# Kernel optimization log

Hardware: AMD Instinct MI355X
Metric: run time of the kernel (lower is better)

## Reference

```python
import jax, jax.numpy as jnp
import numpy as np

NEG_SLOPE = 0.2
EPS = 1e-16


def add_self_loops(edge_index, num_nodes):
    loops = jnp.arange(num_nodes, dtype=edge_index.dtype)
    return jnp.concatenate([edge_index, jnp.stack([loops, loops])], axis=1)


def gat_conv(x, edge_index, W, att_src, att_dst, bias, concat):
    # PyG GATConv: linear -> per-head attention logits -> segment softmax over
    # incoming edges of each destination node -> weighted scatter-add.
    N = x.shape[0]
    H, C = att_src.shape
    ei = add_self_loops(edge_index, N)
    src, dst = ei[0], ei[1]
    h = (x @ W).reshape(N, H, C)                      # [N,H,C]
    a_src = jnp.einsum('nhc,hc->nh', h, att_src)       # [N,H]
    a_dst = jnp.einsum('nhc,hc->nh', h, att_dst)       # [N,H]
    logits = jax.nn.leaky_relu(a_src[src] + a_dst[dst], NEG_SLOPE)  # [E,H]
    m = jax.ops.segment_max(logits, dst, num_segments=N)            # [N,H]
    e = jnp.exp(logits - m[dst])
    s = jax.ops.segment_sum(e, dst, num_segments=N)                 # [N,H]
    alpha = e / (s[dst] + EPS)                                      # [E,H]
    out = jax.ops.segment_sum(h[src] * alpha[:, :, None], dst, num_segments=N)  # [N,H,C]
    out = out.reshape(N, H * C) if concat else out.mean(axis=1)
    return out + bias


def setup_inputs() -> dict:
    key = jax.random.key(0)
    ks = jax.random.split(key, 10)
    N, E, F_in, Hd, heads, F_out = 50000, 800000, 128, 32, 4, 64
    return {
        'x': jax.random.normal(ks[0], (N, F_in), jnp.float32),
        'edge_index': jax.random.randint(ks[1], (2, E), 0, N, jnp.int64),
        'W1': jax.random.normal(ks[2], (F_in, heads * Hd), jnp.float32) * 0.1,
        'att_src1': jax.random.normal(ks[3], (heads, Hd), jnp.float32) * 0.1,
        'att_dst1': jax.random.normal(ks[4], (heads, Hd), jnp.float32) * 0.1,
        'bias1': jax.random.normal(ks[5], (heads * Hd,), jnp.float32) * 0.1,
        'W2': jax.random.normal(ks[6], (heads * Hd, heads * F_out), jnp.float32) * 0.1,
        'att_src2': jax.random.normal(ks[7], (heads, F_out), jnp.float32) * 0.1,
        'att_dst2': jax.random.normal(ks[8], (heads, F_out), jnp.float32) * 0.1,
        'bias2': jax.random.normal(ks[9], (F_out,), jnp.float32) * 0.1,
    }


def reference(x, edge_index, W1, att_src1, att_dst1, bias1, W2, att_src2, att_dst2, bias2):
    h = gat_conv(x, edge_index, W1, att_src1, att_dst1, bias1, concat=True)
    h = jax.nn.elu(h)  # dropout p=0.0 / eval mode -> identity
    out = gat_conv(h, edge_index, W2, att_src2, att_dst2, bias2, concat=False)
    return out
```

## Files before the change

### kernel.cpp

```cpp
#include <hip/hip_runtime.h>

typedef unsigned int uint;
typedef unsigned short ushort;


__device__ __forceinline__ float leaky(float x) { return x >= 0.f ? x : 0.2f * x; }
__device__ __forceinline__ float b2f(ushort h) { return __uint_as_float(((uint)h) << 16); }
__device__ __forceinline__ ushort f2b(float f) {
    uint u = __float_as_uint(f);
    return (ushort)((u + 0x7FFF + ((u >> 16) & 1)) >> 16);
}

#if defined(__has_builtin)
#if __has_builtin(__builtin_amdgcn_fdot2_f32_bf16)
#define HAS_DOT2 1
#endif
#endif
#ifndef HAS_DOT2
#define HAS_DOT2 0
#endif

#if HAS_DOT2
typedef __bf16 bf16v2 __attribute__((ext_vector_type(2)));
__device__ __forceinline__ float dot2bf(uint h2, uint w2, float c) {
    return __builtin_amdgcn_fdot2_f32_bf16(__builtin_bit_cast(bf16v2, h2),
                                           __builtin_bit_cast(bf16v2, w2), c, false);
}
#define DOT2PAIR(hE, hE1, wpk, a0, a1)                                  \
    a0 = dot2bf(__builtin_amdgcn_perm(hE, hE1, 0x01000504), wpk, a0);   \
    a1 = dot2bf(__builtin_amdgcn_perm(hE, hE1, 0x03020706), wpk, a1);
#else
#define DOT2PAIR(hE, hE1, wpk, a0, a1)                                  \
    {                                                                   \
        float wlo = __uint_as_float((wpk) << 16);                       \
        float whi = __uint_as_float((wpk) & 0xffff0000u);               \
        a0 = fmaf(wlo, __uint_as_float((hE) << 16), a0);                \
        a1 = fmaf(wlo, __uint_as_float((hE) & 0xffff0000u), a1);        \
        a0 = fmaf(whi, __uint_as_float((hE1) << 16), a0);               \
        a1 = fmaf(whi, __uint_as_float((hE1) & 0xffff0000u), a1);       \
    }
#endif

__device__ __forceinline__ int detect_bf_local(const void* xin) {
    __shared__ int s_sane;
    if (threadIdx.x == 0) s_sane = 0;
    __syncthreads();
    ushort v = ((const ushort*)xin)[2 * threadIdx.x];
    int ex = (v >> 7) & 0xFF;
    if (v == 0 || (ex >= 100 && ex <= 135)) atomicAdd(&s_sane, 1);
    __syncthreads();
    return s_sane >= 230;
}
__device__ __forceinline__ int detect_is64_local(const int* ei) {
    __shared__ int s_odd;
    if (threadIdx.x == 0) s_odd = 0;
    __syncthreads();
    if (threadIdx.x < 64 && ei[2 * threadIdx.x + 1] != 0) atomicOr(&s_odd, 1);
    __syncthreads();
    return s_odd == 0;
}

__device__ __forceinline__ float rdf(const void* p_, int i, int bf) {
    return bf ? b2f(((const ushort*)p_)[i]) : ((const float*)p_)[i];
}

__device__ __forceinline__ int edge_dst(const int* __restrict__ ei, int E, int e, int is64) {
    return (e >= E) ? (e - E) : (is64 ? ei[2 * E + 2 * e] : ei[E + e]);
}

__global__ void prep_kernel(const void* __restrict__ x, const void* __restrict__ W1,
                            const void* __restrict__ as1, const void* __restrict__ ad1,
                            const void* __restrict__ b1, const void* __restrict__ b2,
                            const void* __restrict__ W2, const void* __restrict__ as2,
                            const void* __restrict__ ad2, const int* __restrict__ ei,
                            int E, int ET,
                            ushort* __restrict__ W1T, float* __restrict__ att1,
                            float* __restrict__ b1f, float* __restrict__ b2f_,
                            float* __restrict__ w2t8, ushort* __restrict__ W2sT,
                            int* __restrict__ flagI, int* __restrict__ flagF,
                            int* __restrict__ bcnt) {
    int b = blockIdx.x, t = threadIdx.x;
    if (b < 64) {
        int bf = detect_bf_local(x);
        int i = b * 256 + t;
        int k = i >> 7, n = i & 127;
        W1T[n * 128 + k] = bf ? ((const ushort*)W1)[i] : f2b(((const float*)W1)[i]);
        return;
    }
    b -= 64;
    if (b == 0) {
        int bf = detect_bf_local(x);
        int is64 = detect_is64_local(ei);
        if (t == 0) { *flagF = bf; *flagI = is64; }
        for (int i = t; i < 512; i += 256) {
            if (i < 128)      att1[i] = rdf(as1, i, bf);
            else if (i < 256) att1[i] = rdf(ad1, i - 128, bf);
            else if (i < 384) b1f[i - 256] = rdf(b1, i - 256, bf);
            else if (i < 448) b2f_[i - 384] = rdf(b2, i - 384, bf);
        }
        return;
    }
    b -= 1;
    if (b < 4) {
        int bf = detect_bf_local(x);
        int idx = b * 256 + t;
        int o = idx >> 7, k = idx & 127, h = o & 3;
        const void* att = (o < 4) ? as2 : ad2;
        float s = 0.f;
        for (int c = 0; c < 64; ++c) s += rdf(W2, k * 256 + h * 64 + c, bf) * rdf(att, h * 64 + c, bf);
        w2t8[o * 128 + k] = s;
        return;
    }
    b -= 4;
    if (b < 128) {
        int bf = detect_bf_local(x);
        int idx = b * 256 + t;
        int c = idx >> 9, hk = idx & 511;
        int h = hk >> 7, k = hk & 127;
        W2sT[c * 512 + hk] = f2b(0.25f * rdf(W2, k * 256 + h * 64 + c, bf));
        return;
    }
    b -= 128;
    {
        int is64 = detect_is64_local(ei);
        __shared__ int bins[256];
        bins[t] = 0;
        __syncthreads();
        int base = b * 4096;
        for (int i = 0; i < 16; ++i) {
            int e = base + i * 256 + t;
            if (e < ET) atomicAdd(&bins[edge_dst(ei, E, e, is64) >> 8], 1);
        }
        __syncthreads();
        if (bins[t]) atomicAdd(&bcnt[t], bins[t]);
    }
}

typedef __attribute__((ext_vector_type(8))) short bf16x8;
typedef __attribute__((ext_vector_type(4))) float floatx4;

__device__ __forceinline__ void gemm1_body(
    int blk, const void* __restrict__ xraw, const int* __restrict__ flagF,
    const ushort* __restrict__ BT, ushort* __restrict__ C,
    const float* __restrict__ att, float4* __restrict__ asrc4, float4* __restrict__ adst4,
    int M) {
    constexpr int K = 128, NT = 8;
    int lane = threadIdx.x & 63, wv = threadIdx.x >> 6;
    int row0 = (blk * 4 + wv) * 16;
    if (row0 >= M) return;
    int m = lane & 15, quad = lane >> 4;
    int rowa = min(row0 + m, M - 1);
    bf16x8 af[4];
    if (*flagF) {
        const bf16x8* arow = (const bf16x8*)((const ushort*)xraw + (size_t)rowa * K);
#pragma unroll
        for (int kk = 0; kk < 4; ++kk) af[kk] = arow[4 * kk + quad];
    } else {
        const float4* arw = (const float4*)((const float*)xraw + (size_t)rowa * K);
#pragma unroll
        for (int kk = 0; kk < 4; ++kk) {
            float4 fa = arw[2 * (4 * kk + quad)];
            float4 fb = arw[2 * (4 * kk + quad) + 1];
            bf16x8 tv;
            tv[0] = (short)f2b(fa.x); tv[1] = (short)f2b(fa.y);
            tv[2] = (short)f2b(fa.z); tv[3] = (short)f2b(fa.w);
            tv[4] = (short)f2b(fb.x); tv[5] = (short)f2b(fb.y);
            tv[6] = (short)f2b(fb.z); tv[7] = (short)f2b(fb.w);
            af[kk] = tv;
        }
    }
    floatx4 acc[NT] = {};
#pragma unroll
    for (int nt = 0; nt < NT; ++nt) {
        const bf16x8* brow = (const bf16x8*)(BT + (size_t)(nt * 16 + m) * K);
#pragma unroll
        for (int kk = 0; kk < 4; ++kk)
            acc[nt] = __builtin_amdgcn_mfma_f32_16x16x32_bf16(af[kk], brow[4 * kk + quad], acc[nt], 0, 0, 0);
    }
#pragma unroll
    for (int nt = 0; nt < NT; ++nt)
#pragma unroll
        for (int r = 0; r < 4; ++r) {
            int row = row0 + quad * 4 + r;
            if (row < M) C[(size_t)row * 128 + nt * 16 + m] = f2b(acc[nt][r]);
        }
    float attS[NT], attD[NT];
#pragma unroll
    for (int nt = 0; nt < NT; ++nt) { attS[nt] = att[nt * 16 + m]; attD[nt] = att[128 + nt * 16 + m]; }
#pragma unroll
    for (int r = 0; r < 4; ++r) {
        float ps[4] = {0, 0, 0, 0}, pd[4] = {0, 0, 0, 0};
#pragma unroll
        for (int nt = 0; nt < NT; ++nt) {
            int h = nt / 2;
            ps[h] = fmaf(acc[nt][r], attS[nt], ps[h]);
            pd[h] = fmaf(acc[nt][r], attD[nt], pd[h]);
        }
#pragma unroll
        for (int off = 1; off < 16; off <<= 1) {
#pragma unroll
            for (int h = 0; h < 4; ++h) {
                ps[h] += __shfl_xor(ps[h], off, 64);
                pd[h] += __shfl_xor(pd[h], off, 64);
            }
        }
        int row = row0 + quad * 4 + r;
        if (m == 0 && row < M) {
            asrc4[row] = make_float4(ps[0], ps[1], ps[2], ps[3]);
            adst4[row] = make_float4(pd[0], pd[1], pd[2], pd[3]);
        }
    }
}

__global__ __launch_bounds__(256) void partg_kernel(
    const int* __restrict__ ei, int E, int ET, const int* __restrict__ flagI,
    const int* __restrict__ bcnt, int* __restrict__ gofs, uint* __restrict__ ebuf,
    int NBUK, int npart,
    const void* __restrict__ xraw, const int* __restrict__ flagF,
    const ushort* __restrict__ BT, ushort* __restrict__ C, const float* __restrict__ att,
    float4* __restrict__ asrc4, float4* __restrict__ adst4, int M) {
    if ((int)blockIdx.x >= npart) {
        gemm1_body(blockIdx.x - npart, xraw, flagF, BT, C, att, asrc4, adst4, M);
        return;
    }
    __shared__ uint stage[8192];
    __shared__ int cnt_s[256], sc[256], sc2[256], lbase[257], cur[256], gb[256];
    int t = threadIdx.x;
    int base = blockIdx.x * 8192;
    cnt_s[t] = 0;
    __syncthreads();
    int is64 = *flagI;
    uint pk[32];
    short bk[32];
#pragma unroll
    for (int i = 0; i < 32; ++i) {
        int e = base + i * 256 + t;
        if (e < ET) {
            int src, dst;
            if (e >= E) { src = dst = e - E; }
            else if (is64) { src = ei[2 * e]; dst = ei[2 * E + 2 * e]; }
            else           { src = ei[e];     dst = ei[E + e]; }
            pk[i] = (uint)src | ((uint)dst << 16);
            bk[i] = (short)(dst >> 8);
            atomicAdd(&cnt_s[bk[i]], 1);
        } else bk[i] = -1;
    }
    __syncthreads();
    int v = cnt_s[t];
    int v2 = (t < NBUK) ? bcnt[t] : 0;
    sc[t] = v;
    sc2[t] = v2;
    __syncthreads();
    for (int off = 1; off < 256; off <<= 1) {
        int a  = (t >= off) ? sc[t - off]  : 0;
        int a2 = (t >= off) ? sc2[t - off] : 0;
        __syncthreads();
        sc[t] += a; sc2[t] += a2;
        __syncthreads();
    }
    lbase[t + 1] = sc[t];
    cur[t] = sc[t] - v;
    int bbx = sc2[t] - v2;
    if (t == 0) lbase[0] = 0;
    __syncthreads();
#pragma unroll
    for (int i = 0; i < 32; ++i)
        if (bk[i] >= 0) {
            int slot = atomicAdd(&cur[bk[i]], 1);
            stage[slot] = pk[i];
        }
    __syncthreads();
    if (t < NBUK) {
        int c = lbase[t + 1] - lbase[t];
        if (c > 0) gb[t] = bbx + atomicAdd(&gofs[t], c);
    }
    __syncthreads();
    int total = lbase[256];
    for (int i = t; i < total; i += 256) {
        int lo = 0, hi = 255;
        while (lo < hi) { int mid = (lo + hi + 1) >> 1; if (lbase[mid] <= i) lo = mid; else hi = mid - 1; }
        ebuf[gb[lo] + (i - lbase[lo])] = stage[i];
    }
}

__global__ __launch_bounds__(256) void bfinal_kernel(const uint* __restrict__ ebuf,
                                                     const int* __restrict__ bcnt,
                                                     int* __restrict__ rowptr,
                                                     int* __restrict__ ecol, int N, int NBUK) {
    __shared__ int hist[2048], cur2[2048], ws[4], bb[256];
    int b = blockIdx.x, t = threadIdx.x;
    int lane = t & 63, wid = t >> 6;
    int d0 = b << 8;
    bb[t] = (t < NBUK) ? bcnt[t] : 0;
#pragma unroll
    for (int j = 0; j < 8; ++j) hist[t * 8 + j] = 0;
    __syncthreads();
    for (int off = 1; off < 256; off <<= 1) {
        int a = (t >= off) ? bb[t - off] : 0;
        __syncthreads();
        bb[t] += a;
        __syncthreads();
    }
    int s = (b == 0) ? 0 : bb[b - 1];
    int e2 = bb[b];
    int total = bb[255];
    for (int i = s + t; i < e2; i += 256) {
        uint pk = ebuf[i];
        int key = (((int)(pk >> 16) - d0) << 3) | (int)((pk & 0xffffu) >> 13);
        atomicAdd(&hist[key], 1);
    }
    __syncthreads();
    int loc[8];
    int v = 0;
#pragma unroll
    for (int j = 0; j < 8; ++j) { loc[j] = v; v += hist[t * 8 + j]; }
    int incl = v;
#pragma unroll
    for (int off = 1; off < 64; off <<= 1) {
        int a = __shfl_up(incl, off, 64);
        if (lane >= off) incl += a;
    }
    if (lane == 63) ws[wid] = incl;
    __syncthreads();
    if (t == 0) {
        int acc = 0;
        for (int j = 0; j < 4; ++j) { int x = ws[j]; ws[j] = acc; acc += x; }
    }
    __syncthreads();
    int excl = incl - v + ws[wid];
    int d = d0 + t;
    if (d < N) rowptr[d] = s + excl;
#pragma unroll
    for (int j = 0; j < 8; ++j) cur2[t * 8 + j] = s + excl + loc[j];
    if (b == NBUK - 1 && t == 0) rowptr[N] = total;
    __syncthreads();
    for (int i = s + t; i < e2; i += 256) {
        uint pk = ebuf[i];
        int key = (((int)(pk >> 16) - d0) << 3) | (int)((pk & 0xffffu) >> 13);
        int pos = atomicAdd(&cur2[key], 1);
        ecol[pos] = (int)(pk & 0xffffu);
    }
}

__global__ void hist_kernel(const int* __restrict__ ei, int E, int N,
                            const int* __restrict__ flag, int* __restrict__ deg) {
    int e = blockIdx.x * blockDim.x + threadIdx.x;
    if (e >= E + N) return;
    atomicAdd(&deg[edge_dst(ei, E, e, *flag)], 1);
}
__global__ void scatter_kernel(const int* __restrict__ ei, int E, int N,
                               const int* __restrict__ flag, const int* __restrict__ rowptr,
                               int* __restrict__ cnt, int* __restrict__ ecol) {
    int e = blockIdx.x * blockDim.x + threadIdx.x;
    if (e >= E + N) return;
    int src, dst;
    if (e >= E) { src = dst = e - E; }
    else if (*flag) { src = ei[2 * e]; dst = ei[2 * E + 2 * e]; }
    else            { src = ei[e];     dst = ei[E + e]; }
    int pos = rowptr[dst] + atomicAdd(&cnt[dst], 1);
    ecol[pos] = src;
}
__global__ __launch_bounds__(1024) void scan1_kernel(const int* __restrict__ deg,
                                                     int* __restrict__ tmp,
                                                     int* __restrict__ bsum, int n) {
    __shared__ int ws[16];
    int tid = threadIdx.x, lane = tid & 63, wid = tid >> 6;
    int i = blockIdx.x * 1024 + tid;
    int v = (i < n) ? deg[i] : 0;
    int incl = v;
#pragma unroll
    for (int off = 1; off < 64; off <<= 1) {
        int t2 = __shfl_up(incl, off, 64);
        if (lane >= off) incl += t2;
    }
    if (lane == 63) ws[wid] = incl;
    __syncthreads();
    if (tid < 16) {
        int wv_ = ws[tid], winc = wv_;
#pragma unroll
        for (int off = 1; off < 16; off <<= 1) {
            int t2 = __shfl_up(winc, off, 16);
            if (tid >= off) winc += t2;
        }
        ws[tid] = winc - wv_;
    }
    __syncthreads();
    int excl = incl - v + ws[wid];
    if (i < n) tmp[i] = excl;
    if (tid == 1023) bsum[blockIdx.x] = excl + v;
}
__global__ void scan2_kernel(int* __restrict__ bsum, int nb) {
    int lane = threadIdx.x;
    int v = (lane < nb) ? bsum[lane] : 0;
    int incl = v;
    for (int off = 1; off < 64; off <<= 1) {
        int t = __shfl_up(incl, off, 64);
        if (lane >= off) incl += t;
    }
    int total = __shfl(incl, nb - 1, 64);
    if (lane < nb) bsum[lane] = incl - v;
    if (lane == 0) bsum[nb] = total;
}
__global__ void scan3_kernel(const int* __restrict__ tmp, const int* __restrict__ bsum,
                             int* __restrict__ rowptr, int* __restrict__ cnt, int n, int nb) {
    int i = blockIdx.x * blockDim.x + threadIdx.x;
    if (i > n) return;
    rowptr[i] = (i == n) ? bsum[nb] : tmp[i] + bsum[i >> 10];
    if (i < n) cnt[i] = 0;
}

__global__ __launch_bounds__(256) void gemm1_kernel(
    const void* __restrict__ xraw, const int* __restrict__ flagF,
    const ushort* __restrict__ BT, ushort* __restrict__ C,
    const float* __restrict__ att, float4* __restrict__ asrc4, float4* __restrict__ adst4, int M) {
    gemm1_body(blockIdx.x, xraw, flagF, BT, C, att, asrc4, adst4, M);
}

__global__ __launch_bounds__(256) void agg1_kernel(
    const ushort* __restrict__ hsrc, const float4* __restrict__ a_src4,
    const float4* __restrict__ a_dst4, const int* __restrict__ rowptr,
    const int* __restrict__ ecol, const float* __restrict__ bias,
    const float* __restrict__ w2t8, uint4* __restrict__ outz,
    float4* __restrict__ asrc2, float4* __restrict__ adst2, int N) {
    constexpr int SH = 7;
    __shared__ __align__(16) ushort elds[4][4][4][20];
    int lane = threadIdx.x & 63, wv = threadIdx.x >> 6;
    int q = lane >> 4, c = lane & 15, qbase = q << 4;
    int n = blockIdx.x * 16 + wv * 4 + q;
    bool nv = n < N;
    int start = 0, end = 0;
    if (nv) { start = rowptr[n]; end = rowptr[n + 1]; }
    int deg = end - start;
    float4 ad = nv ? a_dst4[n] : make_float4(0.f, 0.f, 0.f, 0.f);
    int hh = c >> 2;
    uint laneoff = (uint)c * 8;
    float acc[8] = {};
    float ss0 = 0.f, ss1 = 0.f, ss2 = 0.f, ss3 = 0.f;

    for (int cs = 0; cs < deg; cs += 16) {
        int len = min(16, deg - cs);
        bool v = c < len;
        int sv = v ? ecol[start + cs + c] : 0;
        float4 as = a_src4[sv];
        float e0 = v ? __expf(fminf(leaky(as.x + ad.x), 60.f)) : 0.f;
        float e1 = v ? __expf(fminf(leaky(as.y + ad.y), 60.f)) : 0.f;
        float e2 = v ? __expf(fminf(leaky(as.z + ad.z), 60.f)) : 0.f;
        float e3 = v ? __expf(fminf(leaky(as.w + ad.w), 60.f)) : 0.f;
        ushort r0 = f2b(e0), r1 = f2b(e1), r2 = f2b(e2), r3 = f2b(e3);
        elds[wv][0][q][c] = r0; elds[wv][1][q][c] = r1;
        elds[wv][2][q][c] = r2; elds[wv][3][q][c] = r3;
        ss0 += b2f(r0); ss1 += b2f(r1); ss2 += b2f(r2); ss3 += b2f(r3);
        for (int e = 0; e < len; e += 4) {
            int s0 = __shfl(sv, qbase + e + 0, 64);
            int s1 = __shfl(sv, qbase + e + 1, 64);
            int s2 = __shfl(sv, qbase + e + 2, 64);
            int s3 = __shfl(sv, qbase + e + 3, 64);
            uint2 w = *(const uint2*)&elds[wv][hh][q][e];
            uint4 h0 = *(const uint4*)(hsrc + (((uint)s0) << SH) + laneoff);
            uint4 h1 = *(const uint4*)(hsrc + (((uint)s1) << SH) + laneoff);
            uint4 h2 = *(const uint4*)(hsrc + (((uint)s2) << SH) + laneoff);
            uint4 h3 = *(const uint4*)(hsrc + (((uint)s3) << SH) + laneoff);
            DOT2PAIR(h0.x, h1.x, w.x, acc[0], acc[1]); DOT2PAIR(h0.y, h1.y, w.x, acc[2], acc[3]);
            DOT2PAIR(h0.z, h1.z, w.x, acc[4], acc[5]); DOT2PAIR(h0.w, h1.w, w.x, acc[6], acc[7]);
            DOT2PAIR(h2.x, h3.x, w.y, acc[0], acc[1]); DOT2PAIR(h2.y, h3.y, w.y, acc[2], acc[3]);
            DOT2PAIR(h2.z, h3.z, w.y, acc[4], acc[5]); DOT2PAIR(h2.w, h3.w, w.y, acc[6], acc[7]);
        }
    }
#pragma unroll
    for (int off = 1; off < 16; off <<= 1) {
        ss0 += __shfl_xor(ss0, off, 64); ss1 += __shfl_xor(ss1, off, 64);
        ss2 += __shfl_xor(ss2, off, 64); ss3 += __shfl_xor(ss3, off, 64);
    }
    if (!nv) return;
    float ih = (hh == 0) ? 1.f / (ss0 + 1e-16f) : (hh == 1) ? 1.f / (ss1 + 1e-16f)
             : (hh == 2) ? 1.f / (ss2 + 1e-16f) : 1.f / (ss3 + 1e-16f);
    float4 bA = ((const float4*)bias)[2 * c], bB = ((const float4*)bias)[2 * c + 1];
    float o[8];
    o[0] = acc[0] * ih + bA.x; o[1] = acc[1] * ih + bA.y;
    o[2] = acc[2] * ih + bA.z; o[3] = acc[3] * ih + bA.w;
    o[4] = acc[4] * ih + bB.x; o[5] = acc[5] * ih + bB.y;
    o[6] = acc[6] * ih + bB.z; o[7] = acc[7] * ih + bB.w;
#pragma unroll
    for (int j = 0; j < 8; ++j) o[j] = o[j] > 0.f ? o[j] : __expf(o[j]) - 1.f;
    uint4 pk;
    pk.x = (uint)f2b(o[0]) | ((uint)f2b(o[1]) << 16);
    pk.y = (uint)f2b(o[2]) | ((uint)f2b(o[3]) << 16);
    pk.z = (uint)f2b(o[4]) | ((uint)f2b(o[5]) << 16);
    pk.w = (uint)f2b(o[6]) | ((uint)f2b(o[7]) << 16);
    outz[(size_t)n * 16 + c] = pk;

    float po[8];
#pragma unroll
    for (int oo = 0; oo < 8; ++oo) {
        float4 wA = ((const float4*)(w2t8 + oo * 128))[2 * c];
        float4 wB = ((const float4*)(w2t8 + oo * 128))[2 * c + 1];
        po[oo] = o[0] * wA.x + o[1] * wA.y + o[2] * wA.z + o[3] * wA.w
               + o[4] * wB.x + o[5] * wB.y + o[6] * wB.z + o[7] * wB.w;
    }
#pragma unroll
    for (int off = 1; off < 16; off <<= 1)
#pragma unroll
        for (int oo = 0; oo < 8; ++oo) po[oo] += __shfl_xor(po[oo], off, 64);
    if (c == 0) {
        asrc2[n] = make_float4(po[0], po[1], po[2], po[3]);
        adst2[n] = make_float4(po[4], po[5], po[6], po[7]);
    }
}

__global__ __launch_bounds__(256) void agg2_kernel(
    const ushort* __restrict__ hsrc, const float4* __restrict__ a_src4,
    const float4* __restrict__ a_dst4, const int* __restrict__ rowptr,
    const int* __restrict__ ecol, const ushort* __restrict__ W2sT,
    const float* __restrict__ b2, float* __restrict__ outp, int N) {
    constexpr int SH = 7;
    __shared__ __align__(16) ushort elds[4][4][4][20];
    __shared__ __align__(16) ushort lds_a[16][520];
    int lane = threadIdx.x & 63, wv = threadIdx.x >> 6;
    int q = lane >> 4, c = lane & 15, qbase = q << 4;
    int n = blockIdx.x * 16 + wv * 4 + q;
    bool nv = n < N;
    int start = 0, end = 0;
    if (nv) { start = rowptr[n]; end = rowptr[n + 1]; }
    int deg = end - start;
    float4 ad = nv ? a_dst4[n] : make_float4(0.f, 0.f, 0.f, 0.f);
    uint laneoff = (uint)c * 8;
    float a0_[8] = {}, a1_[8] = {}, a2_[8] = {}, a3_[8] = {};
    float ss0 = 0.f, ss1 = 0.f, ss2 = 0.f, ss3 = 0.f;

    for (int cs = 0; cs < deg; cs += 16) {
        int len = min(16, deg - cs);
        bool v = c < len;
        int sv = v ? ecol[start + cs + c] : 0;
        float4 as = a_src4[sv];
        float e0 = v ? __expf(fminf(leaky(as.x + ad.x), 60.f)) : 0.f;
        float e1 = v ? __expf(fminf(leaky(as.y + ad.y), 60.f)) : 0.f;
        float e2 = v ? __expf(fminf(leaky(as.z + ad.z), 60.f)) : 0.f;
        float e3 = v ? __expf(fminf(leaky(as.w + ad.w), 60.f)) : 0.f;
        ushort r0 = f2b(e0), r1 = f2b(e1), r2 = f2b(e2), r3 = f2b(e3);
        elds[wv][0][q][c] = r0; elds[wv][1][q][c] = r1;
        elds[wv][2][q][c] = r2; elds[wv][3][q][c] = r3;
        ss0 += b2f(r0); ss1 += b2f(r1); ss2 += b2f(r2); ss3 += b2f(r3);
        for (int e = 0; e < len; e += 4) {
            int s0 = __shfl(sv, qbase + e + 0, 64);
            int s1 = __shfl(sv, qbase + e + 1, 64);
            int s2 = __shfl(sv, qbase + e + 2, 64);
            int s3 = __shfl(sv, qbase + e + 3, 64);
            uint2 w0 = *(const uint2*)&elds[wv][0][q][e];
            uint2 w1 = *(const uint2*)&elds[wv][1][q][e];
            uint2 w2 = *(const uint2*)&elds[wv][2][q][e];
            uint2 w3 = *(const uint2*)&elds[wv][3][q][e];
            uint4 h0 = *(const uint4*)(hsrc + (((uint)s0) << SH) + laneoff);
            uint4 h1 = *(const uint4*)(hsrc + (((uint)s1) << SH) + laneoff);
            uint4 h2 = *(const uint4*)(hsrc + (((uint)s2) << SH) + laneoff);
            uint4 h3 = *(const uint4*)(hsrc + (((uint)s3) << SH) + laneoff);
            DOT2PAIR(h0.x, h1.x, w0.x, a0_[0], a0_[1]); DOT2PAIR(h0.y, h1.y, w0.x, a0_[2], a0_[3]);
            DOT2PAIR(h0.z, h1.z, w0.x, a0_[4], a0_[5]); DOT2PAIR(h0.w, h1.w, w0.x, a0_[6], a0_[7]);
            DOT2PAIR(h0.x, h1.x, w1.x, a1_[0], a1_[1]); DOT2PAIR(h0.y, h1.y, w1.x, a1_[2], a1_[3]);
            DOT2PAIR(h0.z, h1.z, w1.x, a1_[4], a1_[5]); DOT2PAIR(h0.w, h1.w, w1.x, a1_[6], a1_[7]);
            DOT2PAIR(h0.x, h1.x, w2.x, a2_[0], a2_[1]); DOT2PAIR(h0.y, h1.y, w2.x, a2_[2], a2_[3]);
            DOT2PAIR(h0.z, h1.z, w2.x, a2_[4], a2_[5]); DOT2PAIR(h0.w, h1.w, w2.x, a2_[6], a2_[7]);
            DOT2PAIR(h0.x, h1.x, w3.x, a3_[0], a3_[1]); DOT2PAIR(h0.y, h1.y, w3.x, a3_[2], a3_[3]);
            DOT2PAIR(h0.z, h1.z, w3.x, a3_[4], a3_[5]); DOT2PAIR(h0.w, h1.w, w3.x, a3_[6], a3_[7]);
            DOT2PAIR(h2.x, h3.x, w0.y, a0_[0], a0_[1]); DOT2PAIR(h2.y, h3.y, w0.y, a0_[2], a0_[3]);
            DOT2PAIR(h2.z, h3.z, w0.y, a0_[4], a0_[5]); DOT2PAIR(h2.w, h3.w, w0.y, a0_[6], a0_[7]);
            DOT2PAIR(h2.x, h3.x, w1.y, a1_[0], a1_[1]); DOT2PAIR(h2.y, h3.y, w1.y, a1_[2], a1_[3]);
            DOT2PAIR(h2.z, h3.z, w1.y, a1_[4], a1_[5]); DOT2PAIR(h2.w, h3.w, w1.y, a1_[6], a1_[7]);
            DOT2PAIR(h2.x, h3.x, w2.y, a2_[0], a2_[1]); DOT2PAIR(h2.y, h3.y, w2.y, a2_[2], a2_[3]);
            DOT2PAIR(h2.z, h3.z, w2.y, a2_[4], a2_[5]); DOT2PAIR(h2.w, h3.w, w2.y, a2_[6], a2_[7]);
            DOT2PAIR(h2.x, h3.x, w3.y, a3_[0], a3_[1]); DOT2PAIR(h2.y, h3.y, w3.y, a3_[2], a3_[3]);
            DOT2PAIR(h2.z, h3.z, w3.y, a3_[4], a3_[5]); DOT2PAIR(h2.w, h3.w, w3.y, a3_[6], a3_[7]);
        }
    }
#pragma unroll
    for (int off = 1; off < 16; off <<= 1) {
        ss0 += __shfl_xor(ss0, off, 64); ss1 += __shfl_xor(ss1, off, 64);
        ss2 += __shfl_xor(ss2, off, 64); ss3 += __shfl_xor(ss3, off, 64);
    }
    float i0 = 1.f / (ss0 + 1e-16f), i1 = 1.f / (ss1 + 1e-16f);
    float i2 = 1.f / (ss2 + 1e-16f), i3 = 1.f / (ss3 + 1e-16f);
    int slot = wv * 4 + q;
    uint4 pk;
    pk.x = (uint)f2b(a0_[0] * i0) | ((uint)f2b(a0_[1] * i0) << 16);
    pk.y = (uint)f2b(a0_[2] * i0) | ((uint)f2b(a0_[3] * i0) << 16);
    pk.z = (uint)f2b(a0_[4] * i0) | ((uint)f2b(a0_[5] * i0) << 16);
    pk.w = (uint)f2b(a0_[6] * i0) | ((uint)f2b(a0_[7] * i0) << 16);
    *(uint4*)&lds_a[slot][0 * 128 + 8 * c] = pk;
    pk.x = (uint)f2b(a1_[0] * i1) | ((uint)f2b(a1_[1] * i1) << 16);
    pk.y = (uint)f2b(a1_[2] * i1) | ((uint)f2b(a1_[3] * i1) << 16);
    pk.z = (uint)f2b(a1_[4] * i1) | ((uint)f2b(a1_[5] * i1) << 16);
    pk.w = (uint)f2b(a1_[6] * i1) | ((uint)f2b(a1_[7] * i1) << 16);
    *(uint4*)&lds_a[slot][1 * 128 + 8 * c] = pk;
    pk.x = (uint)f2b(a2_[0] * i2) | ((uint)f2b(a2_[1] * i2) << 16);
    pk.y = (uint)f2b(a2_[2] * i2) | ((uint)f2b(a2_[3] * i2) << 16);
    pk.z = (uint)f2b(a2_[4] * i2) | ((uint)f2b(a2_[5] * i2) << 16);
    pk.w = (uint)f2b(a2_[6] * i2) | ((uint)f2b(a2_[7] * i2) << 16);
    *(uint4*)&lds_a[slot][2 * 128 + 8 * c] = pk;
    pk.x = (uint)f2b(a3_[0] * i3) | ((uint)f2b(a3_[1] * i3) << 16);
    pk.y = (uint)f2b(a3_[2] * i3) | ((uint)f2b(a3_[3] * i3) << 16);
    pk.z = (uint)f2b(a3_[4] * i3) | ((uint)f2b(a3_[5] * i3) << 16);
    pk.w = (uint)f2b(a3_[6] * i3) | ((uint)f2b(a3_[7] * i3) << 16);
    *(uint4*)&lds_a[slot][3 * 128 + 8 * c] = pk;
    __syncthreads();

    int m = lane & 15, quad = lane >> 4;
    const bf16x8* arow = (const bf16x8*)&lds_a[m][0];
    const bf16x8* brow = (const bf16x8*)(W2sT + (size_t)(wv * 16 + m) * 512);
    floatx4 acc2 = {};
#pragma unroll
    for (int kk = 0; kk < 16; ++kk)
        acc2 = __builtin_amdgcn_mfma_f32_16x16x32_bf16(arow[4 * kk + quad], brow[4 * kk + quad], acc2, 0, 0, 0);
    float bb = b2[wv * 16 + m];
#pragma unroll
    for (int r = 0; r < 4; ++r) {
        int row = quad * 4 + r;
        int node = blockIdx.x * 16 + row;
        if (node < N) outp[(size_t)node * 64 + wv * 16 + m] = acc2[r] + bb;
    }
}

extern "C" void kernel_launch(void* const* d_in, const int* in_sizes, int n_in,
                              void* d_out, int out_size, void* d_ws, size_t ws_size,
                              hipStream_t stream) {
    const void* x_raw = d_in[0];
    const int*  ei    = (const int*)d_in[1];
    const void* W1_p  = d_in[2];
    const void* as1_p = d_in[3];
    const void* ad1_p = d_in[4];
    const void* b1_p  = d_in[5];
    const void* W2_p  = d_in[6];
    const void* as2_p = d_in[7];
    const void* ad2_p = d_in[8];
    const void* b2_p  = d_in[9];

    const int F_IN = 128;
    const int N = in_sizes[0] / F_IN;
    const int E = in_sizes[1] / 2;
    const int ET = E + N;
    const int NB = (N + 1023) / 1024;
    const int NBUK = (N + 255) >> 8;
    const int NBH = (ET + 4095) / 4096;

    char* p = (char*)d_ws;
    auto alloc = [&](size_t bytes) { char* r = p; p += (bytes + 255) & ~(size_t)255; return r; };
    ushort* W1T   = (ushort*)alloc(128 * 128 * 2);
    ushort* W2sT  = (ushort*)alloc(64 * 512 * 2);
    float*  att1f = (float*)alloc(256 * 4);
    float*  w2t8  = (float*)alloc(8 * 128 * 4);
    float*  b1f   = (float*)alloc(128 * 4);
    float*  b2f   = (float*)alloc(64 * 4);
    ushort* h1    = (ushort*)alloc((size_t)N * 128 * 2);
    ushort* hL1   = (ushort*)alloc((size_t)N * 128 * 2);
    float*  asrc1 = (float*)alloc((size_t)N * 4 * 4);
    float*  adst1 = (float*)alloc((size_t)N * 4 * 4);
    float*  asrc2 = (float*)alloc((size_t)N * 4 * 4);
    float*  adst2 = (float*)alloc((size_t)N * 4 * 4);
    int* deg    = (int*)alloc((size_t)N * 4);
    int* cnt    = (int*)alloc((size_t)N * 4);
    int* tmp    = (int*)alloc((size_t)N * 4);
    int* bsum   = (int*)alloc(128 * 4);
    int* rowptr = (int*)alloc((size_t)(N + 1) * 4);
    int* ecol   = (int*)alloc((size_t)ET * 4);
    uint* ebuf  = (uint*)alloc((size_t)ET * 4);
    int* bcnt   = (int*)alloc(256 * 4);
    int* gofs   = (int*)alloc(256 * 4);
    int* flagI  = (int*)alloc(256);
    int* flagF  = (int*)alloc(256);

    hipMemsetAsync(bcnt, 0, 2 * 256 * 4, stream);
    prep_kernel<<<64 + 1 + 4 + 128 + NBH, 256, 0, stream>>>(
        x_raw, W1_p, as1_p, ad1_p, b1_p, b2_p, W2_p, as2_p, ad2_p, ei, E, ET,
        W1T, att1f, b1f, b2f, w2t8, W2sT, flagI, flagF, bcnt);

    int gblocks = (N + 63) / 64;
    if (N <= 65536) {
        int npart = (ET + 8191) / 8192;
        partg_kernel<<<npart + gblocks, 256, 0, stream>>>(
            ei, E, ET, flagI, bcnt, gofs, ebuf, NBUK, npart,
            x_raw, flagF, W1T, h1, att1f, (float4*)asrc1, (float4*)adst1, N);
        bfinal_kernel<<<NBUK, 256, 0, stream>>>(ebuf, bcnt, rowptr, ecol, N, NBUK);
    } else {
        hipMemsetAsync(deg, 0, (size_t)N * 4, stream);
        int eblocks = (ET + 255) / 256;
        hist_kernel<<<eblocks, 256, 0, stream>>>(ei, E, N, flagI, deg);
        scan1_kernel<<<NB, 1024, 0, stream>>>(deg, tmp, bsum, N);
        scan2_kernel<<<1, 64, 0, stream>>>(bsum, NB);
        scan3_kernel<<<(N + 256) / 256, 256, 0, stream>>>(tmp, bsum, rowptr, cnt, N, NB);
        scatter_kernel<<<eblocks, 256, 0, stream>>>(ei, E, N, flagI, rowptr, cnt, ecol);
        gemm1_kernel<<<gblocks, 256, 0, stream>>>(
            x_raw, flagF, W1T, h1, att1f, (float4*)asrc1, (float4*)adst1, N);
    }

    int nblocks16 = (N + 15) / 16;
    agg1_kernel<<<nblocks16, 256, 0, stream>>>(
        h1, (const float4*)asrc1, (const float4*)adst1, rowptr, ecol, b1f, w2t8,
        (uint4*)hL1, (float4*)asrc2, (float4*)adst2, N);
    agg2_kernel<<<nblocks16, 256, 0, stream>>>(
        hL1, (const float4*)asrc2, (const float4*)adst2, rowptr, ecol, W2sT, b2f,
        (float*)d_out, N);
}
```

Baseline: 179.4 us.

## Group destination nodes by degree bucket to balance aggregation wavefronts

The CSR build kernel now counting-sorts the nodes in each 256-node bucket into eight degree classes (degree/16, capped at 7) and writes the permutation to a node-order array. Both aggregation kernels read their destination node through this permutation, so the four nodes handled by one wavefront have similar degrees and less time is lost to divergent loop trip counts. The fallback path writes an identity order. This adds an indirection on the node index and scattered output writes, which cost locality.

```diff
diff --git a/kernel.cpp b/kernel.cpp
--- a/kernel.cpp
+++ b/kernel.cpp
@@ -286,14 +286,18 @@
 __global__ __launch_bounds__(256) void bfinal_kernel(const uint* __restrict__ ebuf,
                                                      const int* __restrict__ bcnt,
                                                      int* __restrict__ rowptr,
-                                                     int* __restrict__ ecol, int N, int NBUK) {
+                                                     int* __restrict__ ecol,
+                                                     int* __restrict__ nodeord,
+                                                     int N, int NBUK) {
     __shared__ int hist[2048], cur2[2048], ws[4], bb[256];
+    __shared__ int kh[8], kbs[8];
     int b = blockIdx.x, t = threadIdx.x;
     int lane = t & 63, wid = t >> 6;
     int d0 = b << 8;
     bb[t] = (t < NBUK) ? bcnt[t] : 0;
 #pragma unroll
     for (int j = 0; j < 8; ++j) hist[t * 8 + j] = 0;
+    if (t < 8) kh[t] = 0;
     __syncthreads();
     for (int off = 1; off < 256; off <<= 1) {
         int a = (t >= off) ? bb[t - off] : 0;
@@ -329,7 +333,8 @@
     __syncthreads();
     int excl = incl - v + ws[wid];
     int d = d0 + t;
-    if (d < N) rowptr[d] = s + excl;
+    bool dvalid = d < N;
+    if (dvalid) rowptr[d] = s + excl;
 #pragma unroll
     for (int j = 0; j < 8; ++j) cur2[t * 8 + j] = s + excl + loc[j];
     if (b == NBUK - 1 && t == 0) rowptr[N] = total;
@@ -339,6 +344,18 @@
         int key = (((int)(pk >> 16) - d0) << 3) | (int)((pk & 0xffffu) >> 13);
         int pos = atomicAdd(&cur2[key], 1);
         ecol[pos] = (int)(pk & 0xffffu);
+    }
+    int dkey = dvalid ? min(v >> 4, 7) : 0;
+    if (dvalid) atomicAdd(&kh[dkey], 1);
+    __syncthreads();
+    if (t == 0) {
+        int acc = 0;
+        for (int j = 0; j < 8; ++j) { int x = kh[j]; kbs[j] = acc; acc += x; kh[j] = 0; }
+    }
+    __syncthreads();
+    if (dvalid) {
+        int r = kbs[dkey] + atomicAdd(&kh[dkey], 1);
+        nodeord[d0 + r] = d;
     }
 }
 
@@ -402,11 +419,12 @@
     if (lane == 0) bsum[nb] = total;
 }
 __global__ void scan3_kernel(const int* __restrict__ tmp, const int* __restrict__ bsum,
-                             int* __restrict__ rowptr, int* __restrict__ cnt, int n, int nb) {
+                             int* __restrict__ rowptr, int* __restrict__ cnt,
+                             int* __restrict__ nodeord, int n, int nb) {
     int i = blockIdx.x * blockDim.x + threadIdx.x;
     if (i > n) return;
     rowptr[i] = (i == n) ? bsum[nb] : tmp[i] + bsum[i >> 10];
-    if (i < n) cnt[i] = 0;
+    if (i < n) { cnt[i] = 0; nodeord[i] = i; }
 }
 
 __global__ __launch_bounds__(256) void gemm1_kernel(
@@ -419,15 +437,16 @@
 __global__ __launch_bounds__(256) void agg1_kernel(
     const ushort* __restrict__ hsrc, const float4* __restrict__ a_src4,
     const float4* __restrict__ a_dst4, const int* __restrict__ rowptr,
-    const int* __restrict__ ecol, const float* __restrict__ bias,
-    const float* __restrict__ w2t8, uint4* __restrict__ outz,
-    float4* __restrict__ asrc2, float4* __restrict__ adst2, int N) {
+    const int* __restrict__ ecol, const int* __restrict__ nodeord,
+    const float* __restrict__ bias, const float* __restrict__ w2t8,
+    uint4* __restrict__ outz, float4* __restrict__ asrc2, float4* __restrict__ adst2, int N) {
     constexpr int SH = 7;
     __shared__ __align__(16) ushort elds[4][4][4][20];
     int lane = threadIdx.x & 63, wv = threadIdx.x >> 6;
     int q = lane >> 4, c = lane & 15, qbase = q << 4;
-    int n = blockIdx.x * 16 + wv * 4 + q;
-    bool nv = n < N;
+    int gid = blockIdx.x * 16 + wv * 4 + q;
+    bool nv = gid < N;
+    int n = nv ? nodeord[gid] : 0;
     int start = 0, end = 0;
     if (nv) { start = rowptr[n]; end = rowptr[n + 1]; }
     int deg = end - start;
@@ -510,15 +529,22 @@
 __global__ __launch_bounds__(256) void agg2_kernel(
     const ushort* __restrict__ hsrc, const float4* __restrict__ a_src4,
     const float4* __restrict__ a_dst4, const int* __restrict__ rowptr,
-    const int* __restrict__ ecol, const ushort* __restrict__ W2sT,
-    const float* __restrict__ b2, float* __restrict__ outp, int N) {
+    const int* __restrict__ ecol, const int* __restrict__ nodeord,
+    const ushort* __restrict__ W2sT, const float* __restrict__ b2,
+    float* __restrict__ outp, int N) {
     constexpr int SH = 7;
     __shared__ __align__(16) ushort elds[4][4][4][20];
     __shared__ __align__(16) ushort lds_a[16][520];
+    __shared__ int nlds[16];
     int lane = threadIdx.x & 63, wv = threadIdx.x >> 6;
     int q = lane >> 4, c = lane & 15, qbase = q << 4;
-    int n = blockIdx.x * 16 + wv * 4 + q;
-    bool nv = n < N;
+    int gid = blockIdx.x * 16 + wv * 4 + q;
+    bool nv = gid < N;
+    int n = nv ? nodeord[gid] : 0;
+    if (threadIdx.x < 16) {
+        int g2 = blockIdx.x * 16 + threadIdx.x;
+        nlds[threadIdx.x] = (g2 < N) ? nodeord[g2] : -1;
+    }
     int start = 0, end = 0;
     if (nv) { start = rowptr[n]; end = rowptr[n + 1]; }
     int deg = end - start;
@@ -613,8 +639,8 @@
 #pragma unroll
     for (int r = 0; r < 4; ++r) {
         int row = quad * 4 + r;
-        int node = blockIdx.x * 16 + row;
-        if (node < N) outp[(size_t)node * 64 + wv * 16 + m] = acc2[r] + bb;
+        int nd = nlds[row];
+        if (nd >= 0) outp[(size_t)nd * 64 + wv * 16 + m] = acc2[r] + bb;
     }
 }
 
@@ -654,6 +680,7 @@
     float*  adst1 = (float*)alloc((size_t)N * 4 * 4);
     float*  asrc2 = (float*)alloc((size_t)N * 4 * 4);
     float*  adst2 = (float*)alloc((size_t)N * 4 * 4);
+    int* nodeord = (int*)alloc((size_t)N * 4);
     int* deg    = (int*)alloc((size_t)N * 4);
     int* cnt    = (int*)alloc((size_t)N * 4);
     int* tmp    = (int*)alloc((size_t)N * 4);
@@ -677,14 +704,14 @@
         partg_kernel<<<npart + gblocks, 256, 0, stream>>>(
             ei, E, ET, flagI, bcnt, gofs, ebuf, NBUK, npart,
             x_raw, flagF, W1T, h1, att1f, (float4*)asrc1, (float4*)adst1, N);
-        bfinal_kernel<<<NBUK, 256, 0, stream>>>(ebuf, bcnt, rowptr, ecol, N, NBUK);
+        bfinal_kernel<<<NBUK, 256, 0, stream>>>(ebuf, bcnt, rowptr, ecol, nodeord, N, NBUK);
     } else {
         hipMemsetAsync(deg, 0, (size_t)N * 4, stream);
         int eblocks = (ET + 255) / 256;
         hist_kernel<<<eblocks, 256, 0, stream>>>(ei, E, N, flagI, deg);
         scan1_kernel<<<NB, 1024, 0, stream>>>(deg, tmp, bsum, N);
         scan2_kernel<<<1, 64, 0, stream>>>(bsum, NB);
-        scan3_kernel<<<(N + 256) / 256, 256, 0, stream>>>(tmp, bsum, rowptr, cnt, N, NB);
+        scan3_kernel<<<(N + 256) / 256, 256, 0, stream>>>(tmp, bsum, rowptr, cnt, nodeord, N, NB);
         scatter_kernel<<<eblocks, 256, 0, stream>>>(ei, E, N, flagI, rowptr, cnt, ecol);
         gemm1_kernel<<<gblocks, 256, 0, stream>>>(
             x_raw, flagF, W1T, h1, att1f, (float4*)asrc1, (float4*)adst1, N);
@@ -692,9 +719,9 @@
 
     int nblocks16 = (N + 15) / 16;
     agg1_kernel<<<nblocks16, 256, 0, stream>>>(
-        h1, (const float4*)asrc1, (const float4*)adst1, rowptr, ecol, b1f, w2t8,
+        h1, (const float4*)asrc1, (const float4*)adst1, rowptr, ecol, nodeord, b1f, w2t8,
         (uint4*)hL1, (float4*)asrc2, (float4*)adst2, N);
     agg2_kernel<<<nblocks16, 256, 0, stream>>>(
-        hL1, (const float4*)asrc2, (const float4*)adst2, rowptr, ecol, W2sT, b2f,
+        hL1, (const float4*)asrc2, (const float4*)adst2, rowptr, ecol, nodeord, W2sT, b2f,
         (float*)d_out, N);
 }
```

After: 183.1 us. 2.1% more time.
